# Kernel tuning notes

Hardware: AMD Instinct MI355X
Metric: run time of the kernel (lower is better)

## Reference

```python
import jax, jax.numpy as jnp
import numpy as np

# Grid / problem sizes (full-res grid for sp_tensor_1; sp_tensor_2 lives on the half-res grid
# and its indices are multiplied by 2 in forward, so they land on even full-res coords).
B, Z, Y, X = 2, 21, 400, 352
Z2, Y2, X2 = 11, 200, 176
N1, N2 = 160000, 60000
CIN, COUT = 64, 128
EPS = 1e-3  # BatchNorm eps


def _build_rulebook():
    """Precompute the SubMConv3d rulebook (spconv builds this once per indice_key).
    Returns padded gather/scatter index arrays for the 26 non-center taps and N.
    Padding uses index N (a dummy zero row / dropped output row)."""
    rng = np.random.default_rng(0)
    # sp_tensor_2: unique voxels on half-res grid, coords scaled by 2 (as done in forward)
    lin2 = rng.choice(B * Z2 * Y2 * X2, size=N2, replace=False)
    b2 = lin2 // (Z2 * Y2 * X2); r = lin2 % (Z2 * Y2 * X2)
    z2 = r // (Y2 * X2); r = r % (Y2 * X2); y2 = r // X2; x2 = r % X2
    c2 = np.stack([b2, 2 * z2, 2 * y2, 2 * x2], 1).astype(np.int64)
    key2 = ((c2[:, 0] * Z + c2[:, 1]) * Y + c2[:, 2]) * X + c2[:, 3]
    # sp_tensor_1: unique voxels on full-res grid, disjoint from scaled sp2 voxels
    lin1 = rng.choice(B * Z * Y * X, size=N1 + 20000, replace=False)
    lin1 = lin1[~np.isin(lin1, key2)][:N1].astype(np.int64)
    b1 = lin1 // (Z * Y * X); r = lin1 % (Z * Y * X)
    z1 = r // (Y * X); r = r % (Y * X); y1 = r // X; x1 = r % X
    c1 = np.stack([b1, z1, y1, x1], 1)
    coords = np.concatenate([c1, c2], 0)  # [N,4] -- sp1 rows first, matching feature concat
    N = coords.shape[0]
    keys = ((coords[:, 0] * Z + coords[:, 1]) * Y + coords[:, 2]) * X + coords[:, 3]
    order = np.argsort(keys); skeys = keys[order]
    gathers, scatters = [], []
    for dz in (-1, 0, 1):
        for dy in (-1, 0, 1):
            for dx in (-1, 0, 1):
                if dz == 0 and dy == 0 and dx == 0:
                    continue  # center tap handled as a dense identity-indexed GEMM
                q = coords[:, 1:] + np.array([dz, dy, dx])
                valid = (q >= 0).all(1) & (q[:, 0] < Z) & (q[:, 1] < Y) & (q[:, 2] < X)
                qk = ((coords[:, 0] * Z + q[:, 0]) * Y + q[:, 1]) * X + q[:, 2]
                pos = np.clip(np.searchsorted(skeys, qk), 0, N - 1)
                hit = valid & (skeys[pos] == qk)
                gathers.append(order[pos[hit]])
                scatters.append(np.nonzero(hit)[0])
    Pmax = max(len(g) for g in gathers)
    G = np.full((26, Pmax), N, np.int32)
    S = np.full((26, Pmax), N, np.int32)
    for i, (g, s) in enumerate(zip(gathers, scatters)):
        G[i, :len(g)] = g
        S[i, :len(s)] = s
    return G, S, N


def setup_inputs() -> dict:
    G, S, N = _build_rulebook()
    k1, k2, k3, k4 = jax.random.split(jax.random.key(0), 4)
    return {
        "features1": jax.random.normal(k1, (N1, CIN), jnp.float32),
        "features2": jax.random.normal(k2, (N - N1, CIN), jnp.float32),
        "weight": jax.random.normal(k3, (27, CIN, COUT), jnp.float32) * (1.0 / np.sqrt(27 * CIN)),
        "bias": jax.random.normal(k4, (COUT,), jnp.float32) * 0.01,
        "gamma": jnp.ones((COUT,), jnp.float32),
        "beta": jnp.zeros((COUT,), jnp.float32),
        "gather_idx": jnp.asarray(G),
        "scatter_idx": jnp.asarray(S),
    }


def reference(features1, features2, weight, bias, gamma, beta, gather_idx, scatter_idx):
    # forward(): concat features of both sparse tensors along the voxel axis
    feats = jnp.concatenate([features1, features2], axis=0)  # [N, Cin]
    N = feats.shape[0]
    # SubMConv3d via gather-GEMM-scatter over the precomputed rulebook.
    # Center tap (kernel index 13): every output voxel pairs with itself -> dense GEMM.
    out = feats @ weight[13] + bias  # [N, Cout]
    # dummy row N absorbs padded rulebook entries
    out = jnp.concatenate([out, jnp.zeros((1, out.shape[1]), out.dtype)], axis=0)
    feats_pad = jnp.concatenate([feats, jnp.zeros((1, feats.shape[1]), feats.dtype)], axis=0)
    taps = [k for k in range(27) if k != 13]
    for i, k in enumerate(taps):
        msg = feats_pad[gather_idx[i]] @ weight[k]  # [Pmax, Cout]
        out = out.at[scatter_idx[i]].add(msg)
    out = out[:N]
    # BatchNorm1d (training mode: batch statistics, biased variance) + ReLU
    mean = jnp.mean(out, axis=0)
    var = jnp.var(out, axis=0)
    out = (out - mean) * jax.lax.rsqrt(var + EPS) * gamma + beta
    return jax.nn.relu(out)
```

## Files before the change

### kernel.cpp

```cpp
#include <hip/hip_runtime.h>

#define EPS 1e-3f

typedef __attribute__((ext_vector_type(8))) short bf8_t;
typedef __attribute__((ext_vector_type(4))) float f32x4;

static __device__ __forceinline__ unsigned f2bf_pack(float a, float b) {
  union { float f; unsigned u; } ca, cb;
  ca.f = a; cb.f = b;
  unsigned ra = (ca.u + 0x7FFFu + ((ca.u >> 16) & 1u)) >> 16;
  unsigned rb = (cb.u + 0x7FFFu + ((cb.u >> 16) & 1u)) >> 16;
  return ra | (rb << 16);
}
static __device__ __forceinline__ unsigned short f2bf1(float x) {
  union { float f; unsigned u; } c; c.f = x;
  return (unsigned short)((c.u + 0x7FFFu + ((c.u >> 16) & 1u)) >> 16);
}
static __device__ __forceinline__ float bf2f(unsigned bits16) {
  union { unsigned u; float f; } c;
  c.u = bits16 << 16;
  return c.f;
}


__global__ __launch_bounds__(256) void to_bf16(
    const float* __restrict__ f1, const float* __restrict__ f2,
    unsigned short* __restrict__ fbuf, int N1, int N) {
  int idx = blockIdx.x * 256 + threadIdx.x;
  if (idx >= (N + 1) * 8) return;
  int row = idx >> 3, seg = idx & 7;
  uint4 o = make_uint4(0, 0, 0, 0);
  if (row < N) {
    const float* src = (row < N1) ? (f1 + (size_t)row * 64)
                                  : (f2 + (size_t)(row - N1) * 64);
    float4 v0 = *(const float4*)(src + seg * 8);
    float4 v1 = *(const float4*)(src + seg * 8 + 4);
    o.x = f2bf_pack(v0.x, v0.y); o.y = f2bf_pack(v0.z, v0.w);
    o.z = f2bf_pack(v1.x, v1.y); o.w = f2bf_pack(v1.z, v1.w);
  }
  *(uint4*)(fbuf + (size_t)idx * 8) = o;
}

__global__ __launch_bounds__(256) void wconv(
    const float* __restrict__ W, unsigned short* __restrict__ Wb) {
  int idx = blockIdx.x * 256 + threadIdx.x;
  int k = idx & 63, n = (idx >> 6) & 127, t = idx >> 13;
  Wb[idx] = f2bf1(W[((size_t)t * 64 + k) * 128 + n]);
}

__global__ __launch_bounds__(256) void scatter_R(
    const int* __restrict__ S, int* __restrict__ R, int N, int pm) {
  const int p = blockIdx.x * 256 + threadIdx.x;
  const int i = blockIdx.y;
  if (p >= pm) return;
  const int idx = i * pm + p;
  const int s = S[idx];
  if (s < N) R[(size_t)s * 26 + i] = idx;
}

__global__ __launch_bounds__(256) void center_mfma(
    const unsigned short* __restrict__ fbuf,
    const unsigned short* __restrict__ Wb13,
    const float* __restrict__ bias,
    unsigned short* __restrict__ outb, int N) {
  __shared__ unsigned short A[128 * 64];
  const int tid = threadIdx.x;
  const int row0 = blockIdx.x * 128;

#pragma unroll
  for (int it = 0; it < 4; ++it) {
    int flat = it * 256 + tid;
    int r = flat >> 3, qs = flat & 7;
    int g = row0 + r; if (g >= N) g = N;
    uint4 v = *(const uint4*)(fbuf + (size_t)g * 64 + qs * 8);
    int rt = r >> 4, m = r & 15, c = qs >> 2, qq = qs & 3;
    *(uint4*)(A + ((rt * 2 + c) * 64 + qq * 16 + m) * 8) = v;
  }
  __syncthreads();

  const int wave = tid >> 6, lane = tid & 63;
  const int ncol = lane & 15, q2 = lane >> 4;
  bf8_t Bf[2][2];
  float bs[2];
#pragma unroll
  for (int ct = 0; ct < 2; ++ct) {
    int col = wave * 32 + ct * 16 + ncol;
    bs[ct] = bias[col];
#pragma unroll
    for (int c = 0; c < 2; ++c)
      Bf[ct][c] = *(const bf8_t*)(Wb13 + (size_t)col * 64 + c * 32 + q2 * 8);
  }
  f32x4 acc[8][2];
#pragma unroll
  for (int rt = 0; rt < 8; ++rt)
#pragma unroll
    for (int ct = 0; ct < 2; ++ct) acc[rt][ct] = (f32x4){0.f, 0.f, 0.f, 0.f};

#pragma unroll
  for (int rt = 0; rt < 8; ++rt) {
    bf8_t a0 = *(const bf8_t*)(A + ((rt * 2 + 0) * 64 + lane) * 8);
    bf8_t a1 = *(const bf8_t*)(A + ((rt * 2 + 1) * 64 + lane) * 8);
#pragma unroll
    for (int ct = 0; ct < 2; ++ct) {
      acc[rt][ct] = __builtin_amdgcn_mfma_f32_16x16x32_bf16(a0, Bf[ct][0], acc[rt][ct], 0, 0, 0);
      acc[rt][ct] = __builtin_amdgcn_mfma_f32_16x16x32_bf16(a1, Bf[ct][1], acc[rt][ct], 0, 0, 0);
    }
  }

#pragma unroll
  for (int rt = 0; rt < 8; ++rt)
#pragma unroll
    for (int ct = 0; ct < 2; ++ct) {
      int col = wave * 32 + ct * 16 + ncol;
#pragma unroll
      for (int e = 0; e < 4; ++e) {
        int row = row0 + rt * 16 + q2 * 4 + e;
        if (row < N)
          outb[(size_t)row * 128 + col] = f2bf1(acc[rt][ct][e] + bs[ct]);
      }
    }
}

__global__ __launch_bounds__(256) void msg_mfma(
    const unsigned short* __restrict__ fbuf,
    const unsigned short* __restrict__ Wb,
    const int* __restrict__ G,
    unsigned short* __restrict__ msgbuf, int N, int pm) {
  const int tap = blockIdx.y;
  const int ktap = tap + (tap >= 13 ? 1 : 0);
  const unsigned short* Wt = Wb + (size_t)ktap * 128 * 64;
  const int* Gi = G + (size_t)tap * pm;
  const int p0 = blockIdx.x * 128;
  if (Gi[p0] >= N) return;

  __shared__ unsigned short A[128 * 64];
  __shared__ int g_lds[128];
  const int tid = threadIdx.x;
  if (tid < 128) {
    int p = p0 + tid;
    g_lds[tid] = (p < pm) ? Gi[p] : N;
  }
  __syncthreads();

#pragma unroll
  for (int it = 0; it < 4; ++it) {
    int flat = it * 256 + tid;
    int r = flat >> 3, qs = flat & 7;
    int g = g_lds[r];
    uint4 v = *(const uint4*)(fbuf + (size_t)g * 64 + qs * 8);
    int rt = r >> 4, m = r & 15, c = qs >> 2, qq = qs & 3;
    *(uint4*)(A + ((rt * 2 + c) * 64 + qq * 16 + m) * 8) = v;
  }
  __syncthreads();

  const int wave = tid >> 6, lane = tid & 63;
  const int ncol = lane & 15, q2 = lane >> 4;
  bf8_t Bf[2][2];
#pragma unroll
  for (int ct = 0; ct < 2; ++ct) {
    int col = wave * 32 + ct * 16 + ncol;
#pragma unroll
    for (int c = 0; c < 2; ++c)
      Bf[ct][c] = *(const bf8_t*)(Wt + (size_t)col * 64 + c * 32 + q2 * 8);
  }
  f32x4 acc[8][2];
#pragma unroll
  for (int rt = 0; rt < 8; ++rt)
#pragma unroll
    for (int ct = 0; ct < 2; ++ct) acc[rt][ct] = (f32x4){0.f, 0.f, 0.f, 0.f};

#pragma unroll
  for (int rt = 0; rt < 8; ++rt) {
    bf8_t a0 = *(const bf8_t*)(A + ((rt * 2 + 0) * 64 + lane) * 8);
    bf8_t a1 = *(const bf8_t*)(A + ((rt * 2 + 1) * 64 + lane) * 8);
#pragma unroll
    for (int ct = 0; ct < 2; ++ct) {
      acc[rt][ct] = __builtin_amdgcn_mfma_f32_16x16x32_bf16(a0, Bf[ct][0], acc[rt][ct], 0, 0, 0);
      acc[rt][ct] = __builtin_amdgcn_mfma_f32_16x16x32_bf16(a1, Bf[ct][1], acc[rt][ct], 0, 0, 0);
    }
  }

#pragma unroll
  for (int rt = 0; rt < 8; ++rt)
#pragma unroll
    for (int ct = 0; ct < 2; ++ct) {
      int col = wave * 32 + ct * 16 + ncol;
#pragma unroll
      for (int e = 0; e < 4; ++e) {
        int p = p0 + rt * 16 + q2 * 4 + e;
        if (p < pm)
          msgbuf[((size_t)tap * pm + p) * 128 + col] = f2bf1(acc[rt][ct][e]);
      }
    }
}

__global__ __launch_bounds__(256) void combine_b(
    unsigned short* __restrict__ outb, const int* __restrict__ R,
    const unsigned short* __restrict__ msgbuf, float* __restrict__ ws,
    int N) {
  const int tid = threadIdx.x;
  const int grp = tid >> 5, l = tid & 31;
  const int base = tid & 32;
  float4 s = make_float4(0.f, 0.f, 0.f, 0.f);
  float4 q = make_float4(0.f, 0.f, 0.f, 0.f);

  for (int j = blockIdx.x * 8 + grp; j < N; j += gridDim.x * 8) {
    uint2 ov = ((const uint2*)(outb + (size_t)j * 128))[l];
    float4 v;
    v.x = bf2f(ov.x & 0xffffu); v.y = bf2f(ov.x >> 16);
    v.z = bf2f(ov.y & 0xffffu); v.w = bf2f(ov.y >> 16);
    int r = (l < 26) ? R[(size_t)j * 26 + l] : -1;
    unsigned long long bal = __ballot(r >= 0);
    unsigned mym = (unsigned)((bal >> base) & 0x3FFFFFFull);
    const bool any = (mym != 0);
    while (mym) {
      int b = __builtin_ctz(mym);
      mym &= mym - 1;
      int ptr = __shfl(r, base + b, 64);
      uint2 mv = ((const uint2*)(msgbuf + (size_t)ptr * 128))[l];
      v.x += bf2f(mv.x & 0xffffu); v.y += bf2f(mv.x >> 16);
      v.z += bf2f(mv.y & 0xffffu); v.w += bf2f(mv.y >> 16);
    }
    if (any) {
      uint2 pk;
      pk.x = f2bf_pack(v.x, v.y); pk.y = f2bf_pack(v.z, v.w);
      ((uint2*)(outb + (size_t)j * 128))[l] = pk;
    }
    s.x += v.x; s.y += v.y; s.z += v.z; s.w += v.w;
    q.x += v.x * v.x; q.y += v.y * v.y; q.z += v.z * v.z; q.w += v.w * v.w;
  }

  __shared__ float red[8 * 32 * 9];
  float* my = red + (grp * 32 + l) * 9;
  my[0] = s.x; my[1] = s.y; my[2] = s.z; my[3] = s.w;
  my[4] = q.x; my[5] = q.y; my[6] = q.z; my[7] = q.w;
  __syncthreads();
  {
    int c4 = tid & 31, jj = tid >> 5;
    float v = 0.f;
#pragma unroll
    for (int g = 0; g < 8; ++g) v += red[(g * 32 + c4) * 9 + jj];
    int col = c4 * 4 + (jj & 3);
    unsafeAtomicAdd(&ws[(jj >> 2) * 4096 + col * 16], v);
  }
}

__global__ __launch_bounds__(256) void norm_b(
    const unsigned short* __restrict__ outb, float* __restrict__ out,
    const float* __restrict__ ws, const float* __restrict__ gamma,
    const float* __restrict__ beta, int total8, float invN) {
  const int tid0 = blockIdx.x * 256 + threadIdx.x;
  const int c0 = (tid0 & 15) * 8;
  float sc[8], sh[8];
#pragma unroll
  for (int k = 0; k < 8; ++k) {
    float m = ws[(c0 + k) * 16] * invN;
    float var = ws[4096 + (c0 + k) * 16] * invN - m * m;
    sc[k] = gamma[c0 + k] * rsqrtf(var + EPS);
    sh[k] = beta[c0 + k] - m * sc[k];
  }
  for (int idx = tid0; idx < total8; idx += gridDim.x * 256) {
    uint4 v = *(const uint4*)(outb + (size_t)idx * 8);
    float f0 = bf2f(v.x & 0xffffu), f1 = bf2f(v.x >> 16);
    float f2 = bf2f(v.y & 0xffffu), f3 = bf2f(v.y >> 16);
    float f4 = bf2f(v.z & 0xffffu), f5 = bf2f(v.z >> 16);
    float f6 = bf2f(v.w & 0xffffu), f7 = bf2f(v.w >> 16);
    float4 o0, o1;
    o0.x = fmaxf(f0 * sc[0] + sh[0], 0.f);
    o0.y = fmaxf(f1 * sc[1] + sh[1], 0.f);
    o0.z = fmaxf(f2 * sc[2] + sh[2], 0.f);
    o0.w = fmaxf(f3 * sc[3] + sh[3], 0.f);
    o1.x = fmaxf(f4 * sc[4] + sh[4], 0.f);
    o1.y = fmaxf(f5 * sc[5] + sh[5], 0.f);
    o1.z = fmaxf(f6 * sc[6] + sh[6], 0.f);
    o1.w = fmaxf(f7 * sc[7] + sh[7], 0.f);
    *(float4*)(out + (size_t)idx * 8) = o0;
    *(float4*)(out + (size_t)idx * 8 + 4) = o1;
  }
}


__global__ __launch_bounds__(256) void center_gemm(
    const float* __restrict__ f1, const float* __restrict__ f2,
    const float* __restrict__ W, const float* __restrict__ bias,
    float* __restrict__ out, int N, int N1) {
  __shared__ float fLDS[128 * 65];
  __shared__ float wLDS[32 * 128];
  const int tid = threadIdx.x;
  const int tx = tid & 15, ty = tid >> 4;
  const int row0 = blockIdx.x * 128;

  for (int k = 0; k < 8; ++k) {
    int flat4 = tid + k * 256;
    int row = flat4 >> 4, c4 = flat4 & 15;
    int grow = row0 + row;
    float4 v = make_float4(0.f, 0.f, 0.f, 0.f);
    if (grow < N) {
      const float* src = (grow < N1) ? (f1 + (size_t)grow * 64)
                                     : (f2 + (size_t)(grow - N1) * 64);
      v = *(const float4*)(src + c4 * 4);
    }
    int l = row * 65 + c4 * 4;
    fLDS[l + 0] = v.x; fLDS[l + 1] = v.y; fLDS[l + 2] = v.z; fLDS[l + 3] = v.w;
  }
  float acc[8][8];
#pragma unroll
  for (int r = 0; r < 8; ++r)
#pragma unroll
    for (int j = 0; j < 8; ++j) acc[r][j] = 0.f;
  for (int kk = 0; kk < 64; kk += 32) {
    __syncthreads();
    for (int k = 0; k < 4; ++k) {
      int flat4 = tid + k * 256;
      int c = flat4 >> 5, col4 = flat4 & 31;
      float4 v = *(const float4*)(W + (size_t)(kk + c) * 128 + col4 * 4);
      *(float4*)(wLDS + c * 128 + col4 * 4) = v;
    }
    __syncthreads();
#pragma unroll 4
    for (int c = 0; c < 32; ++c) {
      float a[8];
#pragma unroll
      for (int r = 0; r < 8; ++r) a[r] = fLDS[(ty * 8 + r) * 65 + kk + c];
      float4 b0 = *(const float4*)(wLDS + c * 128 + tx * 8);
      float4 b1 = *(const float4*)(wLDS + c * 128 + tx * 8 + 4);
      float b[8] = {b0.x, b0.y, b0.z, b0.w, b1.x, b1.y, b1.z, b1.w};
#pragma unroll
      for (int r = 0; r < 8; ++r)
#pragma unroll
        for (int j = 0; j < 8; ++j) acc[r][j] += a[r] * b[j];
    }
  }
  float4 bi0 = *(const float4*)(bias + tx * 8);
  float4 bi1 = *(const float4*)(bias + tx * 8 + 4);
#pragma unroll
  for (int r = 0; r < 8; ++r) {
    int grow = row0 + ty * 8 + r;
    if (grow < N) {
      float4 o0 = make_float4(acc[r][0] + bi0.x, acc[r][1] + bi0.y,
                              acc[r][2] + bi0.z, acc[r][3] + bi0.w);
      float4 o1 = make_float4(acc[r][4] + bi1.x, acc[r][5] + bi1.y,
                              acc[r][6] + bi1.z, acc[r][7] + bi1.w);
      float* dst = out + (size_t)grow * 128 + tx * 8;
      *(float4*)dst = o0;
      *(float4*)(dst + 4) = o1;
    }
  }
}

__global__ __launch_bounds__(256) void msg_gemm_buf(
    const float* __restrict__ f1, const float* __restrict__ f2,
    const float* __restrict__ W27, const int* __restrict__ G,
    const int* __restrict__ S, unsigned short* __restrict__ msgbuf,
    int N, int N1, int pm) {
  const int i = blockIdx.y;
  const int ktap = i + (i >= 13 ? 1 : 0);
  const float* W = W27 + (size_t)ktap * 64 * 128;
  const int* Gi = G + (size_t)i * pm;
  const int* Si = S + (size_t)i * pm;
  const int p0 = blockIdx.x * 128;
  if (Si[p0] >= N) return;
  __shared__ float fLDS[128 * 65];
  __shared__ float wLDS[32 * 128];
  const int tid = threadIdx.x;
  const int tx = tid & 15, ty = tid >> 4;
  for (int k = 0; k < 8; ++k) {
    int flat4 = tid + k * 256;
    int row = flat4 >> 4, c4 = flat4 & 15;
    int p = p0 + row;
    float4 v = make_float4(0.f, 0.f, 0.f, 0.f);
    if (p < pm) {
      int g = Gi[p];
      if (g < N) {
        const float* src = (g < N1) ? (f1 + (size_t)g * 64)
                                    : (f2 + (size_t)(g - N1) * 64);
        v = *(const float4*)(src + c4 * 4);
      }
    }
    int l = row * 65 + c4 * 4;
    fLDS[l + 0] = v.x; fLDS[l + 1] = v.y; fLDS[l + 2] = v.z; fLDS[l + 3] = v.w;
  }
  float acc[8][8];
#pragma unroll
  for (int r = 0; r < 8; ++r)
#pragma unroll
    for (int j = 0; j < 8; ++j) acc[r][j] = 0.f;
  for (int kk = 0; kk < 64; kk += 32) {
    __syncthreads();
    for (int k = 0; k < 4; ++k) {
      int flat4 = tid + k * 256;
      int c = flat4 >> 5, col4 = flat4 & 31;
      float4 v = *(const float4*)(W + (size_t)(kk + c) * 128 + col4 * 4);
      *(float4*)(wLDS + c * 128 + col4 * 4) = v;
    }
    __syncthreads();
#pragma unroll 4
    for (int c = 0; c < 32; ++c) {
      float a[8];
#pragma unroll
      for (int r = 0; r < 8; ++r) a[r] = fLDS[(ty * 8 + r) * 65 + kk + c];
      float4 b0 = *(const float4*)(wLDS + c * 128 + tx * 8);
      float4 b1 = *(const float4*)(wLDS + c * 128 + tx * 8 + 4);
      float b[8] = {b0.x, b0.y, b0.z, b0.w, b1.x, b1.y, b1.z, b1.w};
#pragma unroll
      for (int r = 0; r < 8; ++r)
#pragma unroll
        for (int j = 0; j < 8; ++j) acc[r][j] += a[r] * b[j];
    }
  }
#pragma unroll
  for (int r = 0; r < 8; ++r) {
    int p = p0 + ty * 8 + r;
    if (p < pm) {
      uint4 pk;
      pk.x = f2bf_pack(acc[r][0], acc[r][1]);
      pk.y = f2bf_pack(acc[r][2], acc[r][3]);
      pk.z = f2bf_pack(acc[r][4], acc[r][5]);
      pk.w = f2bf_pack(acc[r][6], acc[r][7]);
      *(uint4*)(msgbuf + ((size_t)i * pm + p) * 128 + tx * 8) = pk;
    }
  }
}

__global__ __launch_bounds__(256) void msg_gemm(
    const float* __restrict__ f1, const float* __restrict__ f2,
    const float* __restrict__ W27, const int* __restrict__ G,
    const int* __restrict__ S, float* __restrict__ out,
    int N, int N1, int pm) {
  const int i = blockIdx.y;
  const int ktap = i + (i >= 13 ? 1 : 0);
  const float* W = W27 + (size_t)ktap * 64 * 128;
  const int* Gi = G + (size_t)i * pm;
  const int* Si = S + (size_t)i * pm;
  const int p0 = blockIdx.x * 128;
  if (Si[p0] >= N) return;
  __shared__ float fLDS[128 * 65];
  __shared__ float wLDS[32 * 128];
  const int tid = threadIdx.x;
  const int tx = tid & 15, ty = tid >> 4;
  for (int k = 0; k < 8; ++k) {
    int flat4 = tid + k * 256;
    int row = flat4 >> 4, c4 = flat4 & 15;
    int p = p0 + row;
    float4 v = make_float4(0.f, 0.f, 0.f, 0.f);
    if (p < pm) {
      int g = Gi[p];
      if (g < N) {
        const float* src = (g < N1) ? (f1 + (size_t)g * 64)
                                    : (f2 + (size_t)(g - N1) * 64);
        v = *(const float4*)(src + c4 * 4);
      }
    }
    int l = row * 65 + c4 * 4;
    fLDS[l + 0] = v.x; fLDS[l + 1] = v.y; fLDS[l + 2] = v.z; fLDS[l + 3] = v.w;
  }
  float acc[8][8];
#pragma unroll
  for (int r = 0; r < 8; ++r)
#pragma unroll
    for (int j = 0; j < 8; ++j) acc[r][j] = 0.f;
  for (int kk = 0; kk < 64; kk += 32) {
    __syncthreads();
    for (int k = 0; k < 4; ++k) {
      int flat4 = tid + k * 256;
      int c = flat4 >> 5, col4 = flat4 & 31;
      float4 v = *(const float4*)(W + (size_t)(kk + c) * 128 + col4 * 4);
      *(float4*)(wLDS + c * 128 + col4 * 4) = v;
    }
    __syncthreads();
#pragma unroll 4
    for (int c = 0; c < 32; ++c) {
      float a[8];
#pragma unroll
      for (int r = 0; r < 8; ++r) a[r] = fLDS[(ty * 8 + r) * 65 + kk + c];
      float4 b0 = *(const float4*)(wLDS + c * 128 + tx * 8);
      float4 b1 = *(const float4*)(wLDS + c * 128 + tx * 8 + 4);
      float b[8] = {b0.x, b0.y, b0.z, b0.w, b1.x, b1.y, b1.z, b1.w};
#pragma unroll
      for (int r = 0; r < 8; ++r)
#pragma unroll
        for (int j = 0; j < 8; ++j) acc[r][j] += a[r] * b[j];
    }
  }
#pragma unroll
  for (int r = 0; r < 8; ++r) {
    int p = p0 + ty * 8 + r;
    if (p < pm) {
      int s = Si[p];
      if (s < N) {
        float* dst = out + (size_t)s * 128 + tx * 8;
#pragma unroll
        for (int j = 0; j < 8; ++j) unsafeAtomicAdd(dst + j, acc[r][j]);
      }
    }
  }
}

__global__ __launch_bounds__(256) void combine_stats(
    float* __restrict__ out, const int* __restrict__ R,
    const unsigned short* __restrict__ msgbuf, float* __restrict__ ws,
    int N) {
  const int tid = threadIdx.x;
  const int grp = tid >> 5, l = tid & 31;
  const int base = tid & 32;
  float4 s = make_float4(0.f, 0.f, 0.f, 0.f);
  float4 q = make_float4(0.f, 0.f, 0.f, 0.f);
  for (int j = blockIdx.x * 8 + grp; j < N; j += gridDim.x * 8) {
    float4 v = ((const float4*)(out + (size_t)j * 128))[l];
    int r = (l < 26) ? R[(size_t)j * 26 + l] : -1;
    unsigned long long bal = __ballot(r >= 0);
    unsigned mym = (unsigned)((bal >> base) & 0x3FFFFFFull);
    const bool any = (mym != 0);
    while (mym) {
      int b = __builtin_ctz(mym);
      mym &= mym - 1;
      int ptr = __shfl(r, base + b, 64);
      uint2 mv = ((const uint2*)(msgbuf + (size_t)ptr * 128))[l];
      v.x += bf2f(mv.x & 0xffffu);
      v.y += bf2f(mv.x >> 16);
      v.z += bf2f(mv.y & 0xffffu);
      v.w += bf2f(mv.y >> 16);
    }
    if (any) ((float4*)(out + (size_t)j * 128))[l] = v;
    s.x += v.x; s.y += v.y; s.z += v.z; s.w += v.w;
    q.x += v.x * v.x; q.y += v.y * v.y; q.z += v.z * v.z; q.w += v.w * v.w;
  }
  __shared__ float red[8 * 32 * 8];
  float* my = red + (grp * 32 + l) * 8;
  my[0] = s.x; my[1] = s.y; my[2] = s.z; my[3] = s.w;
  my[4] = q.x; my[5] = q.y; my[6] = q.z; my[7] = q.w;
  __syncthreads();
  {
    int c4 = tid & 31, j = tid >> 5;
    float v = 0.f;
#pragma unroll
    for (int g = 0; g < 8; ++g) v += red[(g * 32 + c4) * 8 + j];
    int col = c4 * 4 + (j & 3);
    unsafeAtomicAdd(&ws[col + (j >> 2) * 128], v);
  }
}

__global__ __launch_bounds__(256) void stats_kernel(
    const float* __restrict__ out, float* __restrict__ ws, int total4) {
  const int tid = threadIdx.x;
  float4 s = make_float4(0.f, 0.f, 0.f, 0.f);
  float4 q = make_float4(0.f, 0.f, 0.f, 0.f);
  const float4* o4 = (const float4*)out;
  for (int idx = blockIdx.x * 256 + tid; idx < total4; idx += gridDim.x * 256) {
    float4 v = o4[idx];
    s.x += v.x; s.y += v.y; s.z += v.z; s.w += v.w;
    q.x += v.x * v.x; q.y += v.y * v.y; q.z += v.z * v.z; q.w += v.w * v.w;
  }
  __shared__ float red[8 * 32 * 8];
  const int col4 = tid & 31, grpq = tid >> 5;
  float* my = red + (grpq * 32 + col4) * 8;
  my[0] = s.x; my[1] = s.y; my[2] = s.z; my[3] = s.w;
  my[4] = q.x; my[5] = q.y; my[6] = q.z; my[7] = q.w;
  __syncthreads();
  {
    int c4 = tid & 31, j = tid >> 5;
    float v = 0.f;
#pragma unroll
    for (int g = 0; g < 8; ++g) v += red[(g * 32 + c4) * 8 + j];
    int col = c4 * 4 + (j & 3);
    unsafeAtomicAdd(&ws[col + (j >> 2) * 128], v);
  }
}

__global__ __launch_bounds__(256) void norm_kernel(
    float* __restrict__ out, const float* __restrict__ ws,
    const float* __restrict__ gamma, const float* __restrict__ beta,
    int total4, float invN) {
  const int tid = threadIdx.x;
  const int c4 = tid & 31;
  float4 s = ((const float4*)ws)[c4];
  float4 q = ((const float4*)ws)[32 + c4];
  float4 g = ((const float4*)gamma)[c4];
  float4 b = ((const float4*)beta)[c4];
  float m0 = s.x * invN, m1 = s.y * invN, m2 = s.z * invN, m3 = s.w * invN;
  float sc0 = g.x * rsqrtf(q.x * invN - m0 * m0 + EPS);
  float sc1 = g.y * rsqrtf(q.y * invN - m1 * m1 + EPS);
  float sc2 = g.z * rsqrtf(q.z * invN - m2 * m2 + EPS);
  float sc3 = g.w * rsqrtf(q.w * invN - m3 * m3 + EPS);
  float sh0 = b.x - m0 * sc0, sh1 = b.y - m1 * sc1;
  float sh2 = b.z - m2 * sc2, sh3 = b.w - m3 * sc3;
  float4* o4 = (float4*)out;
  for (int idx = blockIdx.x * 256 + tid; idx < total4; idx += gridDim.x * 256) {
    float4 v = o4[idx];
    v.x = fmaxf(v.x * sc0 + sh0, 0.f);
    v.y = fmaxf(v.y * sc1 + sh1, 0.f);
    v.z = fmaxf(v.z * sc2 + sh2, 0.f);
    v.w = fmaxf(v.w * sc3 + sh3, 0.f);
    o4[idx] = v;
  }
}

extern "C" void kernel_launch(void* const* d_in, const int* in_sizes, int n_in,
                              void* d_out, int out_size, void* d_ws, size_t ws_size,
                              hipStream_t stream) {
  const float* f1 = (const float*)d_in[0];
  const float* f2 = (const float*)d_in[1];
  const float* W = (const float*)d_in[2];
  const float* bias = (const float*)d_in[3];
  const float* gamma = (const float*)d_in[4];
  const float* beta = (const float*)d_in[5];
  const int* G = (const int*)d_in[6];
  const int* S = (const int*)d_in[7];
  const int N1 = in_sizes[0] / 64;
  const int N2 = in_sizes[1] / 64;
  const int N = N1 + N2;
  const int pm = in_sizes[6] / 26;
  float* out = (float*)d_out;
  float* ws = (float*)d_ws;

  const size_t AL = 255;
  const size_t offR = 32768;
  const size_t Rb = (size_t)N * 26 * 4;
  const size_t offF = (offR + Rb + AL) & ~AL;
  const size_t Fb = (size_t)(N + 1) * 64 * 2;
  const size_t offW = (offF + Fb + AL) & ~AL;
  const size_t Wbyt = (size_t)27 * 128 * 64 * 2;
  const size_t offM = (offW + Wbyt + AL) & ~AL;
  const size_t Mb = (size_t)26 * pm * 128 * 2;
  const size_t offO = (offM + Mb + AL) & ~AL;
  const size_t Ob = (size_t)N * 128 * 2;
  const bool full = ws_size >= offO + Ob;

  const size_t offR2 = 1024;
  const size_t offM2 = (offR2 + Rb + AL) & ~AL;
  const bool fast2 = ws_size >= offM2 + Mb;

  if (full) {
    int* R = (int*)((char*)d_ws + offR);
    unsigned short* fbuf = (unsigned short*)((char*)d_ws + offF);
    unsigned short* Wb = (unsigned short*)((char*)d_ws + offW);
    unsigned short* msgbuf = (unsigned short*)((char*)d_ws + offM);
    unsigned short* outb = (unsigned short*)((char*)d_ws + offO);

    (void)hipMemsetAsync(ws, 0, 32768, stream);
    (void)hipMemsetAsync(R, 0xFF, Rb, stream);
    to_bf16<<<((N + 1) * 8 + 255) / 256, 256, 0, stream>>>(f1, f2, fbuf, N1, N);
    wconv<<<(27 * 128 * 64) / 256, 256, 0, stream>>>(W, Wb);
    scatter_R<<<dim3((pm + 255) / 256, 26), 256, 0, stream>>>(S, R, N, pm);

    center_mfma<<<(N + 127) / 128, 256, 0, stream>>>(
        fbuf, Wb + (size_t)13 * 128 * 64, bias, outb, N);
    msg_mfma<<<dim3((pm + 127) / 128, 26), 256, 0, stream>>>(
        fbuf, Wb, G, msgbuf, N, pm);

    combine_b<<<2048, 256, 0, stream>>>(outb, R, msgbuf, ws, N);
    norm_b<<<2048, 256, 0, stream>>>(outb, out, ws, gamma, beta, N * 16,
                                     1.0f / N);
  } else if (fast2) {
    int* R = (int*)((char*)d_ws + offR2);
    unsigned short* msgbuf = (unsigned short*)((char*)d_ws + offM2);
    (void)hipMemsetAsync(ws, 0, 256 * sizeof(float), stream);
    (void)hipMemsetAsync(R, 0xFF, Rb, stream);
    center_gemm<<<(N + 127) / 128, 256, 0, stream>>>(
        f1, f2, W + (size_t)13 * 64 * 128, bias, out, N, N1);
    scatter_R<<<dim3((pm + 255) / 256, 26), 256, 0, stream>>>(S, R, N, pm);
    msg_gemm_buf<<<dim3((pm + 127) / 128, 26), 256, 0, stream>>>(
        f1, f2, W, G, S, msgbuf, N, N1, pm);
    combine_stats<<<1024, 256, 0, stream>>>(out, R, msgbuf, ws, N);
    norm_kernel<<<2048, 256, 0, stream>>>(out, ws, gamma, beta, N * 32,
                                          1.0f / N);
  } else {
    (void)hipMemsetAsync(ws, 0, 256 * sizeof(float), stream);
    center_gemm<<<(N + 127) / 128, 256, 0, stream>>>(
        f1, f2, W + (size_t)13 * 64 * 128, bias, out, N, N1);
    msg_gemm<<<dim3((pm + 127) / 128, 26), 256, 0, stream>>>(
        f1, f2, W, G, S, out, N, N1, pm);
    stats_kernel<<<1024, 256, 0, stream>>>(out, ws, N * 32);
    norm_kernel<<<2048, 256, 0, stream>>>(out, ws, gamma, beta, N * 32,
                                          1.0f / N);
  }
}
```

Baseline: 330.6 us.

## Replace per-voxel tap table with CSR-compacted message buffer for combine

```diff
diff --git a/kernel.cpp b/kernel.cpp
--- a/kernel.cpp
+++ b/kernel.cpp
@@ -48,14 +48,53 @@
   Wb[idx] = f2bf1(W[((size_t)t * 64 + k) * 128 + n]);
 }
 
-__global__ __launch_bounds__(256) void scatter_R(
-    const int* __restrict__ S, int* __restrict__ R, int N, int pm) {
+__global__ __launch_bounds__(256) void count_slots(
+    const int* __restrict__ S, unsigned char* __restrict__ SL,
+    int* __restrict__ cnt, int N, int pm) {
   const int p = blockIdx.x * 256 + threadIdx.x;
   const int i = blockIdx.y;
   if (p >= pm) return;
   const int idx = i * pm + p;
   const int s = S[idx];
-  if (s < N) R[(size_t)s * 26 + i] = idx;
+  if (s < N) SL[idx] = (unsigned char)atomicAdd(&cnt[s], 1);
+}
+
+__global__ __launch_bounds__(256) void prefix_base(
+    const int* __restrict__ cnt, int2* __restrict__ BC,
+    int* __restrict__ gtot, int N) {
+  const int t = threadIdx.x;
+  const int j0 = blockIdx.x * 1024 + t * 4;
+  int c0 = 0, c1 = 0, c2 = 0, c3 = 0;
+  if (j0 + 3 < N) {
+    int4 c = *(const int4*)(cnt + j0);
+    c0 = c.x; c1 = c.y; c2 = c.z; c3 = c.w;
+  } else {
+    if (j0 < N) c0 = cnt[j0];
+    if (j0 + 1 < N) c1 = cnt[j0 + 1];
+    if (j0 + 2 < N) c2 = cnt[j0 + 2];
+  }
+  const int tsum = c0 + c1 + c2 + c3;
+  int incl = tsum;
+#pragma unroll
+  for (int off = 1; off < 64; off <<= 1) {
+    int u = __shfl_up(incl, off, 64);
+    if ((t & 63) >= off) incl += u;
+  }
+  __shared__ int wsum[4];
+  if ((t & 63) == 63) wsum[t >> 6] = incl;
+  __syncthreads();
+  if (t == 0) {
+    int w0 = wsum[0], w1 = wsum[1], w2 = wsum[2], w3 = wsum[3];
+    int gb = atomicAdd(gtot, w0 + w1 + w2 + w3);
+    wsum[0] = gb; wsum[1] = gb + w0;
+    wsum[2] = gb + w0 + w1; wsum[3] = gb + w0 + w1 + w2;
+  }
+  __syncthreads();
+  const int excl = wsum[t >> 6] + incl - tsum;
+  if (j0 < N) BC[j0] = make_int2(excl, c0);
+  if (j0 + 1 < N) BC[j0 + 1] = make_int2(excl + c0, c1);
+  if (j0 + 2 < N) BC[j0 + 2] = make_int2(excl + c0 + c1, c2);
+  if (j0 + 3 < N) BC[j0 + 3] = make_int2(excl + c0 + c1 + c2, c3);
 }
 
 __global__ __launch_bounds__(256) void center_mfma(
@@ -121,24 +160,34 @@
     }
 }
 
-__global__ __launch_bounds__(256) void msg_mfma(
+__global__ __launch_bounds__(256) void msg_mfma_c(
     const unsigned short* __restrict__ fbuf,
     const unsigned short* __restrict__ Wb,
-    const int* __restrict__ G,
-    unsigned short* __restrict__ msgbuf, int N, int pm) {
+    const int* __restrict__ G, const int* __restrict__ S,
+    const int2* __restrict__ BC, const unsigned char* __restrict__ SL,
+    unsigned short* __restrict__ compact, int N, int pm) {
   const int tap = blockIdx.y;
   const int ktap = tap + (tap >= 13 ? 1 : 0);
   const unsigned short* Wt = Wb + (size_t)ktap * 128 * 64;
   const int* Gi = G + (size_t)tap * pm;
+  const int* Si = S + (size_t)tap * pm;
   const int p0 = blockIdx.x * 128;
   if (Gi[p0] >= N) return;
 
   __shared__ unsigned short A[128 * 64];
   __shared__ int g_lds[128];
+  __shared__ int d_lds[128];
   const int tid = threadIdx.x;
   if (tid < 128) {
     int p = p0 + tid;
-    g_lds[tid] = (p < pm) ? Gi[p] : N;
+    int g = N, d = -1;
+    if (p < pm) {
+      g = Gi[p];
+      int s = Si[p];
+      if (s < N) d = BC[s].x + (int)SL[(size_t)tap * pm + p];
+    }
+    g_lds[tid] = g;
+    d_lds[tid] = d;
   }
   __syncthreads();
 
@@ -181,47 +230,42 @@
   }
 
 #pragma unroll
-  for (int rt = 0; rt < 8; ++rt)
+  for (int rt = 0; rt < 8; ++rt) {
+    int dl[4];
+#pragma unroll
+    for (int e = 0; e < 4; ++e) dl[e] = d_lds[rt * 16 + q2 * 4 + e];
 #pragma unroll
     for (int ct = 0; ct < 2; ++ct) {
       int col = wave * 32 + ct * 16 + ncol;
 #pragma unroll
-      for (int e = 0; e < 4; ++e) {
-        int p = p0 + rt * 16 + q2 * 4 + e;
-        if (p < pm)
-          msgbuf[((size_t)tap * pm + p) * 128 + col] = f2bf1(acc[rt][ct][e]);
-      }
-    }
-}
-
-__global__ __launch_bounds__(256) void combine_b(
-    unsigned short* __restrict__ outb, const int* __restrict__ R,
-    const unsigned short* __restrict__ msgbuf, float* __restrict__ ws,
+      for (int e = 0; e < 4; ++e)
+        if (dl[e] >= 0)
+          compact[(size_t)dl[e] * 128 + col] = f2bf1(acc[rt][ct][e]);
+    }
+  }
+}
+
+__global__ __launch_bounds__(256) void combine_c(
+    unsigned short* __restrict__ outb, const int2* __restrict__ BC,
+    const unsigned short* __restrict__ compact, float* __restrict__ ws,
     int N) {
   const int tid = threadIdx.x;
   const int grp = tid >> 5, l = tid & 31;
-  const int base = tid & 32;
   float4 s = make_float4(0.f, 0.f, 0.f, 0.f);
   float4 q = make_float4(0.f, 0.f, 0.f, 0.f);
 
   for (int j = blockIdx.x * 8 + grp; j < N; j += gridDim.x * 8) {
+    int2 bc = BC[j];
     uint2 ov = ((const uint2*)(outb + (size_t)j * 128))[l];
     float4 v;
     v.x = bf2f(ov.x & 0xffffu); v.y = bf2f(ov.x >> 16);
     v.z = bf2f(ov.y & 0xffffu); v.w = bf2f(ov.y >> 16);
-    int r = (l < 26) ? R[(size_t)j * 26 + l] : -1;
-    unsigned long long bal = __ballot(r >= 0);
-    unsigned mym = (unsigned)((bal >> base) & 0x3FFFFFFull);
-    const bool any = (mym != 0);
-    while (mym) {
-      int b = __builtin_ctz(mym);
-      mym &= mym - 1;
-      int ptr = __shfl(r, base + b, 64);
-      uint2 mv = ((const uint2*)(msgbuf + (size_t)ptr * 128))[l];
+    for (int k = 0; k < bc.y; ++k) {
+      uint2 mv = ((const uint2*)(compact + (size_t)(bc.x + k) * 128))[l];
       v.x += bf2f(mv.x & 0xffffu); v.y += bf2f(mv.x >> 16);
       v.z += bf2f(mv.y & 0xffffu); v.w += bf2f(mv.y >> 16);
     }
-    if (any) {
+    if (bc.y) {
       uint2 pk;
       pk.x = f2bf_pack(v.x, v.y); pk.y = f2bf_pack(v.z, v.w);
       ((uint2*)(outb + (size_t)j * 128))[l] = pk;
@@ -279,6 +323,16 @@
   }
 }
 
+
+__global__ __launch_bounds__(256) void scatter_R(
+    const int* __restrict__ S, int* __restrict__ R, int N, int pm) {
+  const int p = blockIdx.x * 256 + threadIdx.x;
+  const int i = blockIdx.y;
+  if (p >= pm) return;
+  const int idx = i * pm + p;
+  const int s = S[idx];
+  if (s < N) R[(size_t)s * 26 + i] = idx;
+}
 
 __global__ __launch_bounds__(256) void center_gemm(
     const float* __restrict__ f1, const float* __restrict__ f2,
@@ -614,9 +668,13 @@
   float* ws = (float*)d_ws;
 
   const size_t AL = 255;
-  const size_t offR = 32768;
-  const size_t Rb = (size_t)N * 26 * 4;
-  const size_t offF = (offR + Rb + AL) & ~AL;
+  const size_t offC = 32768;
+  const size_t Cb = (size_t)N * 4;
+  const size_t offBC = (offC + Cb + AL) & ~AL;
+  const size_t BCb = (size_t)N * 8;
+  const size_t offSL = (offBC + BCb + AL) & ~AL;
+  const size_t SLb = (size_t)26 * pm;
+  const size_t offF = (offSL + SLb + AL) & ~AL;
   const size_t Fb = (size_t)(N + 1) * 64 * 2;
   const size_t offW = (offF + Fb + AL) & ~AL;
   const size_t Wbyt = (size_t)27 * 128 * 64 * 2;
@@ -626,29 +684,34 @@
   const size_t Ob = (size_t)N * 128 * 2;
   const bool full = ws_size >= offO + Ob;
 
+  const size_t Rb = (size_t)N * 26 * 4;
   const size_t offR2 = 1024;
   const size_t offM2 = (offR2 + Rb + AL) & ~AL;
   const bool fast2 = ws_size >= offM2 + Mb;
 
   if (full) {
-    int* R = (int*)((char*)d_ws + offR);
+    int* cnt = (int*)((char*)d_ws + offC);
+    int2* BC = (int2*)((char*)d_ws + offBC);
+    unsigned char* SLp = (unsigned char*)((char*)d_ws + offSL);
     unsigned short* fbuf = (unsigned short*)((char*)d_ws + offF);
     unsigned short* Wb = (unsigned short*)((char*)d_ws + offW);
-    unsigned short* msgbuf = (unsigned short*)((char*)d_ws + offM);
+    unsigned short* compact = (unsigned short*)((char*)d_ws + offM);
     unsigned short* outb = (unsigned short*)((char*)d_ws + offO);
+    int* gtot = (int*)((char*)d_ws + 28672);
 
     (void)hipMemsetAsync(ws, 0, 32768, stream);
-    (void)hipMemsetAsync(R, 0xFF, Rb, stream);
+    (void)hipMemsetAsync(cnt, 0, Cb, stream);
     to_bf16<<<((N + 1) * 8 + 255) / 256, 256, 0, stream>>>(f1, f2, fbuf, N1, N);
     wconv<<<(27 * 128 * 64) / 256, 256, 0, stream>>>(W, Wb);
-    scatter_R<<<dim3((pm + 255) / 256, 26), 256, 0, stream>>>(S, R, N, pm);
+    count_slots<<<dim3((pm + 255) / 256, 26), 256, 0, stream>>>(S, SLp, cnt, N, pm);
+    prefix_base<<<(N + 1023) / 1024, 256, 0, stream>>>(cnt, BC, gtot, N);
 
     center_mfma<<<(N + 127) / 128, 256, 0, stream>>>(
         fbuf, Wb + (size_t)13 * 128 * 64, bias, outb, N);
-    msg_mfma<<<dim3((pm + 127) / 128, 26), 256, 0, stream>>>(
-        fbuf, Wb, G, msgbuf, N, pm);
-
-    combine_b<<<2048, 256, 0, stream>>>(outb, R, msgbuf, ws, N);
+    msg_mfma_c<<<dim3((pm + 127) / 128, 26), 256, 0, stream>>>(
+        fbuf, Wb, G, S, BC, SLp, compact, N, pm);
+
+    combine_c<<<2048, 256, 0, stream>>>(outb, BC, compact, ws, N);
     norm_b<<<2048, 256, 0, stream>>>(outb, out, ws, gamma, beta, N * 16,
                                      1.0f / N);
   } else if (fast2) {
```

New measurement: 334.1 us. No clear change (+1.1%).
